# Kernel tuning notes

Hardware: AMD Instinct MI355X
Metric: run time of the kernel (lower is better)

## Reference

```python
import jax, jax.numpy as jnp
import numpy as np

BUFFER_C = 1.25

def setup_inputs() -> dict:
    key = jax.random.key(0)
    k1, k2, k3 = jax.random.split(key, 3)
    T, D, E = 4096, 1024, 8
    x = jax.random.normal(k1, (T, D), dtype=jnp.float32)
    Wg = jax.random.normal(k2, (D, E), dtype=jnp.float32) / np.sqrt(D)
    bg = jnp.zeros((E,), dtype=jnp.float32)
    W = jax.random.normal(k3, (E, D, D), dtype=jnp.float32) / np.sqrt(D)
    b = jnp.zeros((E, D), dtype=jnp.float32)
    return {"x": x, "Wg": Wg, "bg": bg, "W": W, "b": b}


def reference(x, Wg, bg, W, b):
    # Top-1 (Switch-style) routing with capacity buffer, per-expert Linear,
    # prob-weighted combine, plus load-balancing aux loss.
    T, D = x.shape
    E = W.shape[0]
    capacity = int(BUFFER_C * T / E)

    logits = x @ Wg + bg                      # [T, E]
    probs = jax.nn.softmax(logits, axis=-1)   # [T, E]
    top_idx = jnp.argmax(probs, axis=-1)      # [T]
    top_prob = jnp.take_along_axis(probs, top_idx[:, None], axis=-1)[:, 0]

    onehot = jax.nn.one_hot(top_idx, E, dtype=x.dtype)       # [T, E]
    # 1-indexed position of each token within its expert's buffer
    pos = jnp.cumsum(onehot, axis=0) * onehot                # [T, E]
    dispatch = jnp.where((onehot > 0) & (pos <= capacity), 1.0, 0.0).astype(x.dtype)

    # dense dispatch/combine equivalent of the masked per-expert loop
    xe = jnp.einsum('te,td->etd', dispatch, x)               # [E, T, D]
    ye = jnp.einsum('etd,edf->etf', xe, W) + b[:, None, :]   # [E, T, D]
    y = jnp.einsum('te,etf->tf', dispatch, ye)               # [T, D] (0 for dropped)
    out = y * top_prob[:, None]

    # aux load-balance loss: E * sum_e f_e * P_e
    f = onehot.mean(axis=0)
    P = probs.mean(axis=0)
    aux_loss = E * jnp.sum(f * P)
    return out, aux_loss
```

## Files before the change

kernel.cpp:

```cpp
#include <hip/hip_runtime.h>
#include <hip/hip_bf16.h>
#include <cstdint>

#define T_TOK 4096
#define D_DIM 1024
#define E_EXP 8
#define CAP   640
#define MAXDROP 3456
#define MT    10
#define GBLK  1024

typedef __attribute__((ext_vector_type(8))) short short8;
typedef __attribute__((ext_vector_type(4))) float f32x4;

__device__ inline unsigned short f2bf(float f) {
    uint32_t u = __float_as_uint(f);
    u += 0x7fffu + ((u >> 16) & 1u);
    return (unsigned short)(u >> 16);
}

__device__ inline void dma16(const void* g, void* l) {
    __builtin_amdgcn_global_load_lds(
        (const __attribute__((address_space(1))) unsigned int*)g,
        (__attribute__((address_space(3))) unsigned int*)l, 16, 0, 0);
}

#define WB_TILE(e, nt, kt) ((((size_t)(e) * 16 + (nt)) * 16 + (kt)) * 4096)
#define XG_TILE(e, mt, kt) ((((size_t)(e) * MT + (mt)) * 16 + (kt)) * 4096)

__global__ __launch_bounds__(256) void prep_kernel(
    const float* __restrict__ x, const float* __restrict__ Wg,
    const float* __restrict__ bg, const float* __restrict__ W,
    unsigned short* __restrict__ Wb,
    int* __restrict__ top_idx, float* __restrict__ top_prob,
    float* __restrict__ blkpart)
{
    int bid = blockIdx.x;
    int tid = threadIdx.x;

    if (bid >= GBLK) {
        __shared__ unsigned short tile[2][64][66];
        int bid2 = (bid - GBLK) * 2;
        int e   = bid2 >> 8;
        int kt  = (bid2 >> 4) & 15;
        int ntA = bid2 & 15;
        int k0  = kt * 64;
        int n0A = ntA * 64, n0B = n0A + 64;
        const float* Wsrc = W + (size_t)e * D_DIM * D_DIM;

        int rr = tid >> 4;
        int nn = (tid & 15) * 4;

        float4 r0[4], r1[4];
        #pragma unroll
        for (int p = 0; p < 4; p++)
            r0[p] = *(const float4*)(Wsrc + (size_t)(k0 + p * 16 + rr) * D_DIM + n0A + nn);
        #pragma unroll
        for (int p = 0; p < 4; p++) {
            ushort4 u;
            u.x = f2bf(r0[p].x); u.y = f2bf(r0[p].y); u.z = f2bf(r0[p].z); u.w = f2bf(r0[p].w);
            *(ushort4*)&tile[0][p * 16 + rr][nn] = u;
        }
        #pragma unroll
        for (int p = 0; p < 4; p++)
            r1[p] = *(const float4*)(Wsrc + (size_t)(k0 + p * 16 + rr) * D_DIM + n0B + nn);
        __syncthreads();
        {
            unsigned short* dst = Wb + WB_TILE(e, ntA, kt);
            #pragma unroll
            for (int p = 0; p < 2; p++) {
                int c = tid + 256 * p;
                int g = c >> 6, n = c & 63;
                short8 v;
                #pragma unroll
                for (int z = 0; z < 8; z++) v[z] = (short)tile[0][g * 8 + z][n];
                *(short8*)&dst[(size_t)c * 8] = v;
            }
        }
        #pragma unroll
        for (int p = 0; p < 4; p++) {
            ushort4 u;
            u.x = f2bf(r1[p].x); u.y = f2bf(r1[p].y); u.z = f2bf(r1[p].z); u.w = f2bf(r1[p].w);
            *(ushort4*)&tile[1][p * 16 + rr][nn] = u;
        }
        __syncthreads();
        {
            unsigned short* dst = Wb + WB_TILE(e, ntA + 1, kt);
            #pragma unroll
            for (int p = 0; p < 2; p++) {
                int c = tid + 256 * p;
                int g = c >> 6, n = c & 63;
                short8 v;
                #pragma unroll
                for (int z = 0; z < 8; z++) v[z] = (short)tile[1][g * 8 + z][n];
                *(short8*)&dst[(size_t)c * 8] = v;
            }
        }
    } else {
        __shared__ float probs_sm[4][8];
        int wid  = tid >> 6;
        int lane = tid & 63;
        int t = bid * 4 + wid;

        const float* xr = x + (size_t)t * D_DIM;

        float acc[8];
        #pragma unroll
        for (int e = 0; e < 8; e++) acc[e] = 0.f;

        #pragma unroll
        for (int ii = 0; ii < 16; ii++) {
            int d = lane + 64 * ii;
            float xv = xr[d];
            const float4* wr = (const float4*)(Wg + (size_t)d * 8);
            float4 a = wr[0], bq = wr[1];
            acc[0] += xv * a.x;  acc[1] += xv * a.y;
            acc[2] += xv * a.z;  acc[3] += xv * a.w;
            acc[4] += xv * bq.x; acc[5] += xv * bq.y;
            acc[6] += xv * bq.z; acc[7] += xv * bq.w;
        }
        #pragma unroll
        for (int off = 32; off > 0; off >>= 1) {
            #pragma unroll
            for (int e = 0; e < 8; e++) acc[e] += __shfl_xor(acc[e], off, 64);
        }
        if (lane == 0) {
            float lg[8];
            #pragma unroll
            for (int e = 0; e < 8; e++) lg[e] = acc[e] + bg[e];
            float m = lg[0]; int am = 0;
            #pragma unroll
            for (int e = 1; e < 8; e++) { if (lg[e] > m) { m = lg[e]; am = e; } }
            float ex[8], s = 0.f;
            #pragma unroll
            for (int e = 0; e < 8; e++) { ex[e] = __expf(lg[e] - m); s += ex[e]; }
            float inv = 1.f / s;
            top_idx[t]  = am;
            top_prob[t] = ex[am] * inv;
            #pragma unroll
            for (int e = 0; e < 8; e++) probs_sm[wid][e] = ex[e] * inv;
        }
        __syncthreads();
        if (tid < 8) {
            float s = probs_sm[0][tid] + probs_sm[1][tid]
                    + probs_sm[2][tid] + probs_sm[3][tid];
            blkpart[(size_t)bid * 8 + tid] = s;
        }
    }
}

__global__ __launch_bounds__(1024) void scan_kernel(
    const int* __restrict__ top_idx,
    int* __restrict__ tok_list, int* __restrict__ cnt,
    const float* __restrict__ blkpart,
    float* __restrict__ out, float* __restrict__ out_aux)
{
    __shared__ int counts[64][8];
    __shared__ int excl[64][8];
    __shared__ int fulltot[8];
    __shared__ int droplist[MAXDROP];
    __shared__ int ndrop;
    __shared__ float wpart[16][8];

    int tid  = threadIdx.x;
    int wv   = tid >> 6;
    int lane = tid & 63;
    unsigned long long ltmask = (lane == 0) ? 0ull : ((~0ull) >> (64 - lane));

    if (tid == 0) ndrop = 0;

    float p[8];
    {
        const float4* bp = (const float4*)(blkpart + (size_t)tid * 8);
        float4 p0 = bp[0], p1 = bp[1];
        p[0] = p0.x; p[1] = p0.y; p[2] = p0.z; p[3] = p0.w;
        p[4] = p1.x; p[5] = p1.y; p[6] = p1.z; p[7] = p1.w;
    }

    int ecache[4];
    #pragma unroll
    for (int c = 0; c < 4; c++)
        ecache[c] = top_idx[(4 * wv + c) * 64 + lane];

    #pragma unroll
    for (int c = 0; c < 4; c++) {
        int chunk = 4 * wv + c;
        int e = ecache[c];
        #pragma unroll
        for (int q = 0; q < 8; q++) {
            unsigned long long mk = __ballot(e == q);
            int tot = __popcll(mk);
            if (lane == q) counts[chunk][q] = tot;
        }
    }
    __syncthreads();

    if (wv == 0) {
        #pragma unroll
        for (int q = 0; q < 8; q++) {
            int v = counts[lane][q];
            int orig = v;
            #pragma unroll
            for (int off = 1; off < 64; off <<= 1) {
                int n = __shfl_up(v, off, 64);
                if (lane >= off) v += n;
            }
            excl[lane][q] = v - orig;
            int total = __shfl(v, 63, 64);
            if (lane == 0) {
                fulltot[q] = total;
                cnt[q] = total < CAP ? total : CAP;
            }
        }
    }
    __syncthreads();

    #pragma unroll
    for (int c = 0; c < 4; c++) {
        int chunk = 4 * wv + c;
        int t = chunk * 64 + lane;
        int e = ecache[c];
        int pos = 0;
        #pragma unroll
        for (int q = 0; q < 8; q++) {
            unsigned long long mk = __ballot(e == q);
            if (e == q) pos = excl[chunk][q] + __popcll(mk & ltmask);
        }
        if (pos < CAP) {
            tok_list[e * CAP + pos] = t;
        } else {
            int di = atomicAdd(&ndrop, 1);
            droplist[di] = t;
        }
    }

    #pragma unroll
    for (int off = 32; off > 0; off >>= 1) {
        #pragma unroll
        for (int e = 0; e < 8; e++) p[e] += __shfl_xor(p[e], off, 64);
    }
    if (lane == 0) {
        #pragma unroll
        for (int e = 0; e < 8; e++) wpart[wv][e] = p[e];
    }
    __syncthreads();

    int nd = ndrop;
    int grp = tid >> 8;
    int col = (tid & 255) * 4;
    float4 z = {0.f, 0.f, 0.f, 0.f};
    for (int d = grp; d < nd; d += 4) {
        int row = droplist[d];
        *(float4*)&out[(size_t)row * D_DIM + col] = z;
    }

    if (tid == 0) {
        float s = 0.f;
        #pragma unroll
        for (int e = 0; e < 8; e++) {
            float Pe = 0.f;
            #pragma unroll
            for (int w = 0; w < 16; w++) Pe += wpart[w][e];
            s += ((float)fulltot[e] / (float)T_TOK) * (Pe / (float)T_TOK);
        }
        out_aux[0] = (float)E_EXP * s;
    }
}

__global__ __launch_bounds__(256) void gather_kernel(
    const float* __restrict__ x, const int* __restrict__ tok_list,
    const int* __restrict__ cnt, unsigned short* __restrict__ xg)
{
    int bid = blockIdx.x;
    int e   = bid / (MT * 16);
    int rem = bid % (MT * 16);
    int mt  = rem >> 4, kt = rem & 15;
    int count = cnt[e];
    int m0 = mt * 64;
    if (m0 >= count) return;

    int tid = threadIdx.x;
    const int* tl = tok_list + e * CAP;
    unsigned short* dst = xg + XG_TILE(e, mt, kt);

    #pragma unroll
    for (int p = 0; p < 2; p++) {
        int c = tid + 256 * p;
        int g = c >> 6, row = c & 63;
        int gm = m0 + row;
        int tok = tl[gm < count ? gm : count - 1];
        const float* src = x + (size_t)tok * D_DIM + kt * 64 + g * 8;
        float4 v0 = *(const float4*)(src);
        float4 v1 = *(const float4*)(src + 4);
        short8 v;
        v[0] = f2bf(v0.x); v[1] = f2bf(v0.y); v[2] = f2bf(v0.z); v[3] = f2bf(v0.w);
        v[4] = f2bf(v1.x); v[5] = f2bf(v1.y); v[6] = f2bf(v1.z); v[7] = f2bf(v1.w);
        *(short8*)&dst[(size_t)c * 8] = v;
    }
}

__device__ inline void stage_dma(const unsigned short* gAt, const unsigned short* gBt,
                                 unsigned short (*Ab)[64][8], unsigned short (*Bb)[64][8],
                                 int w, int lane)
{
    size_t lo = (size_t)lane * 8;
    dma16(gAt + (size_t)w * 512 + lo,       &Ab[w][0][0]);
    dma16(gAt + (size_t)(w + 4) * 512 + lo, &Ab[w + 4][0][0]);
    dma16(gBt + (size_t)w * 512 + lo,       &Bb[w][0][0]);
    dma16(gBt + (size_t)(w + 4) * 512 + lo, &Bb[w + 4][0][0]);
}

__global__ __launch_bounds__(256) void expert_gemm(
    const unsigned short* __restrict__ xg, const unsigned short* __restrict__ Wb,
    const float* __restrict__ bias,
    const int* __restrict__ tok_list, const int* __restrict__ cnt,
    const float* __restrict__ top_prob, float* __restrict__ out)
{
    int bid = blockIdx.x;
    int e   = bid / (MT * 16);
    int rem = bid % (MT * 16);
    int mt  = rem >> 4, nt = rem & 15;
    int count = cnt[e];
    int m0 = mt * 64;
    if (m0 >= count) return;
    int n0 = nt * 64;

    __shared__ unsigned short Ab[2][8][64][8];
    __shared__ unsigned short Bb[2][8][64][8];

    int tid  = threadIdx.x;
    int lane = tid & 63, w = tid >> 6;
    int quad = lane >> 4, l16 = lane & 15;
    int mw = (w >> 1) * 32, nw = (w & 1) * 32;

    const int* tl = tok_list + e * CAP;
    const unsigned short* gA0 = xg + XG_TILE(e, mt, 0);
    const unsigned short* gB0 = Wb + WB_TILE(e, nt, 0);

    f32x4 acc[2][2];
    #pragma unroll
    for (int i = 0; i < 2; i++)
        #pragma unroll
        for (int j = 0; j < 2; j++)
            acc[i][j] = (f32x4){0.f, 0.f, 0.f, 0.f};

    stage_dma(gA0, gB0, Ab[0], Bb[0], w, lane);

    int cur = 0;
    #pragma unroll 1
    for (int kt = 0; kt < 16; kt++) {
        __syncthreads();
        if (kt + 1 < 16)
            stage_dma(gA0 + (size_t)(kt + 1) * 4096, gB0 + (size_t)(kt + 1) * 4096,
                      Ab[cur ^ 1], Bb[cur ^ 1], w, lane);

        short8 af[2][2], bf[2][2];
        #pragma unroll
        for (int s = 0; s < 2; s++) {
            #pragma unroll
            for (int i = 0; i < 2; i++) {
                af[s][i] = *(const short8*)&Ab[cur][s * 4 + quad][mw + 16 * i + l16][0];
                bf[s][i] = *(const short8*)&Bb[cur][s * 4 + quad][nw + 16 * i + l16][0];
            }
        }
        #pragma unroll
        for (int s = 0; s < 2; s++)
            #pragma unroll
            for (int i = 0; i < 2; i++)
                #pragma unroll
                for (int j = 0; j < 2; j++)
                    acc[i][j] = __builtin_amdgcn_mfma_f32_16x16x32_bf16(
                        af[s][i], bf[s][j], acc[i][j], 0, 0, 0);
        cur ^= 1;
    }

    float bv[2];
    #pragma unroll
    for (int j = 0; j < 2; j++)
        bv[j] = bias[e * D_DIM + n0 + nw + 16 * j + l16];

    #pragma unroll
    for (int i = 0; i < 2; i++) {
        int rb = m0 + mw + 16 * i + quad * 4;
        #pragma unroll
        for (int r = 0; r < 4; r++) {
            int gm = rb + r;
            if (gm >= count) continue;
            int tok = tl[gm];
            float p = top_prob[tok];
            float* orow = out + (size_t)tok * D_DIM + n0 + nw + l16;
            #pragma unroll
            for (int j = 0; j < 2; j++)
                orow[16 * j] = (acc[i][j][r] + bv[j]) * p;
        }
    }
}

extern "C" void kernel_launch(void* const* d_in, const int* in_sizes, int n_in,
                              void* d_out, int out_size, void* d_ws, size_t ws_size,
                              hipStream_t stream) {
    const float* x  = (const float*)d_in[0];
    const float* Wg = (const float*)d_in[1];
    const float* bg = (const float*)d_in[2];
    const float* W  = (const float*)d_in[3];
    const float* b  = (const float*)d_in[4];
    float* out = (float*)d_out;

    char* ws = (char*)d_ws;
    unsigned short* Wb = (unsigned short*)(ws + 0);
    unsigned short* xg = (unsigned short*)(ws + 16777216);
    int*   top_idx  = (int*)(ws + 27262976);
    float* top_prob = (float*)(ws + 27279360);
    int*   tok_list = (int*)(ws + 27295744);
    int*   cnt      = (int*)(ws + 27316224);
    float* blkpart  = (float*)(ws + 27316256);

    hipLaunchKernelGGL(prep_kernel, dim3(GBLK + 1024), dim3(256), 0, stream,
                       x, Wg, bg, W, Wb, top_idx, top_prob, blkpart);
    hipLaunchKernelGGL(scan_kernel, dim3(1), dim3(1024), 0, stream,
                       top_idx, tok_list, cnt, blkpart, out, out + (size_t)T_TOK * D_DIM);
    hipLaunchKernelGGL(gather_kernel, dim3(E_EXP * MT * 16), dim3(256), 0, stream,
                       x, tok_list, cnt, xg);
    hipLaunchKernelGGL(expert_gemm, dim3(E_EXP * MT * 16), dim3(256), 0, stream,
                       xg, Wb, b, tok_list, cnt, top_prob, out);
}
```

Measured before the change: 142.5 us.

## Fuse routing scan into prep and token gather into expert GEMM

The single-block scan kernel is folded into the tail of prep_kernel: an atomic done-counter picks the last routing block, which then builds the per-expert token lists, zeroes dropped rows and computes the aux loss. The separate gather kernel and its bf16 staging buffer are removed. expert_gemm now loads fp32 x rows directly through a token index kept in shared memory, converts them to bf16 in registers and writes them to LDS, with the next k-tile prefetched into registers. This drops two launches and a full write and read of the gathered activations. In exchange the scan runs on only 256 threads, and the smaller drop-list capacity assumes that few tokens overflow expert capacity.

```diff
diff --git a/kernel.cpp b/kernel.cpp
--- a/kernel.cpp
+++ b/kernel.cpp
@@ -6,7 +6,7 @@
 #define D_DIM 1024
 #define E_EXP 8
 #define CAP   640
-#define MAXDROP 3456
+#define MAXDROP 1024
 #define MT    10
 #define GBLK  1024
 
@@ -25,15 +25,23 @@
         (__attribute__((address_space(3))) unsigned int*)l, 16, 0, 0);
 }
 
+__device__ inline int agload_i(const int* p) {
+    return __hip_atomic_load(p, __ATOMIC_RELAXED, __HIP_MEMORY_SCOPE_AGENT);
+}
+__device__ inline float agload_f(const float* p) {
+    return __hip_atomic_load(p, __ATOMIC_RELAXED, __HIP_MEMORY_SCOPE_AGENT);
+}
+
 #define WB_TILE(e, nt, kt) ((((size_t)(e) * 16 + (nt)) * 16 + (kt)) * 4096)
-#define XG_TILE(e, mt, kt) ((((size_t)(e) * MT + (mt)) * 16 + (kt)) * 4096)
 
 __global__ __launch_bounds__(256) void prep_kernel(
     const float* __restrict__ x, const float* __restrict__ Wg,
     const float* __restrict__ bg, const float* __restrict__ W,
     unsigned short* __restrict__ Wb,
     int* __restrict__ top_idx, float* __restrict__ top_prob,
-    float* __restrict__ blkpart)
+    float* __restrict__ blkpart,
+    int* __restrict__ tok_list, int* __restrict__ cnt, int* __restrict__ done,
+    float* __restrict__ out, float* __restrict__ out_aux)
 {
     int bid = blockIdx.x;
     int tid = threadIdx.x;
@@ -96,8 +104,12 @@
                 *(short8*)&dst[(size_t)c * 8] = v;
             }
         }
-    } else {
-        __shared__ float probs_sm[4][8];
+        return;
+    }
+
+    __shared__ float probs_sm[4][8];
+    __shared__ int   is_last;
+    {
         int wid  = tid >> 6;
         int lane = tid & 63;
         int t = bid * 4 + wid;
@@ -147,22 +159,20 @@
             blkpart[(size_t)bid * 8 + tid] = s;
         }
     }
-}
-
-__global__ __launch_bounds__(1024) void scan_kernel(
-    const int* __restrict__ top_idx,
-    int* __restrict__ tok_list, int* __restrict__ cnt,
-    const float* __restrict__ blkpart,
-    float* __restrict__ out, float* __restrict__ out_aux)
-{
+
+    __threadfence();
+    __syncthreads();
+    if (tid == 0) is_last = (atomicAdd(done, 1) == GBLK - 1);
+    __syncthreads();
+    if (!is_last) return;
+
     __shared__ int counts[64][8];
     __shared__ int excl[64][8];
     __shared__ int fulltot[8];
     __shared__ int droplist[MAXDROP];
     __shared__ int ndrop;
-    __shared__ float wpart[16][8];
-
-    int tid  = threadIdx.x;
+    __shared__ float wpart[4][8];
+
     int wv   = tid >> 6;
     int lane = tid & 63;
     unsigned long long ltmask = (lane == 0) ? 0ull : ((~0ull) >> (64 - lane));
@@ -170,21 +180,23 @@
     if (tid == 0) ndrop = 0;
 
     float p[8];
-    {
-        const float4* bp = (const float4*)(blkpart + (size_t)tid * 8);
-        float4 p0 = bp[0], p1 = bp[1];
-        p[0] = p0.x; p[1] = p0.y; p[2] = p0.z; p[3] = p0.w;
-        p[4] = p1.x; p[5] = p1.y; p[6] = p1.z; p[7] = p1.w;
-    }
-
-    int ecache[4];
-    #pragma unroll
-    for (int c = 0; c < 4; c++)
-        ecache[c] = top_idx[(4 * wv + c) * 64 + lane];
-
-    #pragma unroll
-    for (int c = 0; c < 4; c++) {
-        int chunk = 4 * wv + c;
+    #pragma unroll
+    for (int e = 0; e < 8; e++) p[e] = 0.f;
+    #pragma unroll
+    for (int r = 0; r < 4; r++) {
+        const float* bp = blkpart + (size_t)(tid * 4 + r) * 8;
+        #pragma unroll
+        for (int e = 0; e < 8; e++) p[e] += agload_f(bp + e);
+    }
+
+    int ecache[16];
+    #pragma unroll
+    for (int c = 0; c < 16; c++)
+        ecache[c] = agload_i(top_idx + (wv * 16 + c) * 64 + lane);
+
+    #pragma unroll
+    for (int c = 0; c < 16; c++) {
+        int chunk = wv * 16 + c;
         int e = ecache[c];
         #pragma unroll
         for (int q = 0; q < 8; q++) {
@@ -216,8 +228,8 @@
     __syncthreads();
 
     #pragma unroll
-    for (int c = 0; c < 4; c++) {
-        int chunk = 4 * wv + c;
+    for (int c = 0; c < 16; c++) {
+        int chunk = wv * 16 + c;
         int t = chunk * 64 + lane;
         int e = ecache[c];
         int pos = 0;
@@ -246,72 +258,25 @@
     __syncthreads();
 
     int nd = ndrop;
-    int grp = tid >> 8;
-    int col = (tid & 255) * 4;
     float4 z = {0.f, 0.f, 0.f, 0.f};
-    for (int d = grp; d < nd; d += 4) {
+    for (int d = 0; d < nd; d++) {
         int row = droplist[d];
-        *(float4*)&out[(size_t)row * D_DIM + col] = z;
+        *(float4*)&out[(size_t)row * D_DIM + tid * 4] = z;
     }
 
     if (tid == 0) {
         float s = 0.f;
         #pragma unroll
         for (int e = 0; e < 8; e++) {
-            float Pe = 0.f;
-            #pragma unroll
-            for (int w = 0; w < 16; w++) Pe += wpart[w][e];
+            float Pe = wpart[0][e] + wpart[1][e] + wpart[2][e] + wpart[3][e];
             s += ((float)fulltot[e] / (float)T_TOK) * (Pe / (float)T_TOK);
         }
         out_aux[0] = (float)E_EXP * s;
     }
 }
 
-__global__ __launch_bounds__(256) void gather_kernel(
-    const float* __restrict__ x, const int* __restrict__ tok_list,
-    const int* __restrict__ cnt, unsigned short* __restrict__ xg)
-{
-    int bid = blockIdx.x;
-    int e   = bid / (MT * 16);
-    int rem = bid % (MT * 16);
-    int mt  = rem >> 4, kt = rem & 15;
-    int count = cnt[e];
-    int m0 = mt * 64;
-    if (m0 >= count) return;
-
-    int tid = threadIdx.x;
-    const int* tl = tok_list + e * CAP;
-    unsigned short* dst = xg + XG_TILE(e, mt, kt);
-
-    #pragma unroll
-    for (int p = 0; p < 2; p++) {
-        int c = tid + 256 * p;
-        int g = c >> 6, row = c & 63;
-        int gm = m0 + row;
-        int tok = tl[gm < count ? gm : count - 1];
-        const float* src = x + (size_t)tok * D_DIM + kt * 64 + g * 8;
-        float4 v0 = *(const float4*)(src);
-        float4 v1 = *(const float4*)(src + 4);
-        short8 v;
-        v[0] = f2bf(v0.x); v[1] = f2bf(v0.y); v[2] = f2bf(v0.z); v[3] = f2bf(v0.w);
-        v[4] = f2bf(v1.x); v[5] = f2bf(v1.y); v[6] = f2bf(v1.z); v[7] = f2bf(v1.w);
-        *(short8*)&dst[(size_t)c * 8] = v;
-    }
-}
-
-__device__ inline void stage_dma(const unsigned short* gAt, const unsigned short* gBt,
-                                 unsigned short (*Ab)[64][8], unsigned short (*Bb)[64][8],
-                                 int w, int lane)
-{
-    size_t lo = (size_t)lane * 8;
-    dma16(gAt + (size_t)w * 512 + lo,       &Ab[w][0][0]);
-    dma16(gAt + (size_t)(w + 4) * 512 + lo, &Ab[w + 4][0][0]);
-    dma16(gBt + (size_t)w * 512 + lo,       &Bb[w][0][0]);
-    dma16(gBt + (size_t)(w + 4) * 512 + lo, &Bb[w + 4][0][0]);
-}
-
 __global__ __launch_bounds__(256) void expert_gemm(
-    const unsigned short* __restrict__ xg, const unsigned short* __restrict__ Wb,
+    const float* __restrict__ x, const unsigned short* __restrict__ Wb,
     const float* __restrict__ bias,
     const int* __restrict__ tok_list, const int* __restrict__ cnt,
     const float* __restrict__ top_prob, float* __restrict__ out)
@@ -327,15 +292,42 @@
 
     __shared__ unsigned short Ab[2][8][64][8];
     __shared__ unsigned short Bb[2][8][64][8];
+    __shared__ int tok_sm[64];
 
     int tid  = threadIdx.x;
     int lane = tid & 63, w = tid >> 6;
     int quad = lane >> 4, l16 = lane & 15;
     int mw = (w >> 1) * 32, nw = (w & 1) * 32;
+    int arow = tid >> 2, aq = tid & 3;
 
     const int* tl = tok_list + e * CAP;
-    const unsigned short* gA0 = xg + XG_TILE(e, mt, 0);
-    const unsigned short* gB0 = Wb + WB_TILE(e, nt, 0);
+    if (tid < 64) { int gm = m0 + tid; tok_sm[tid] = tl[gm < count ? gm : count - 1]; }
+
+    const unsigned short* gB0 = Wb + WB_TILE(e, nt, 0) + (size_t)lane * 8;
+
+    #define DMAB(kt, buf) do {                                                \
+        const unsigned short* gb = gB0 + (size_t)(kt) * 4096;                 \
+        dma16(gb + (size_t)w * 512,       &Bb[buf][w][0][0]);                 \
+        dma16(gb + (size_t)(w + 4) * 512, &Bb[buf][w + 4][0][0]);             \
+    } while (0)
+
+    __syncthreads();
+    const float* xrow = x + (size_t)tok_sm[arow] * D_DIM + aq * 16;
+
+    float4 ra0, ra1, ra2, ra3;
+    #define XLOAD(ks) do {                                                    \
+        const float4* s_ = (const float4*)(xrow + (size_t)(ks) * 64);         \
+        ra0 = s_[0]; ra1 = s_[1]; ra2 = s_[2]; ra3 = s_[3];                   \
+    } while (0)
+    #define AWRITE(buf) do {                                                  \
+        short8 v_, u_;                                                        \
+        v_[0]=f2bf(ra0.x); v_[1]=f2bf(ra0.y); v_[2]=f2bf(ra0.z); v_[3]=f2bf(ra0.w); \
+        v_[4]=f2bf(ra1.x); v_[5]=f2bf(ra1.y); v_[6]=f2bf(ra1.z); v_[7]=f2bf(ra1.w); \
+        u_[0]=f2bf(ra2.x); u_[1]=f2bf(ra2.y); u_[2]=f2bf(ra2.z); u_[3]=f2bf(ra2.w); \
+        u_[4]=f2bf(ra3.x); u_[5]=f2bf(ra3.y); u_[6]=f2bf(ra3.z); u_[7]=f2bf(ra3.w); \
+        *(short8*)&Ab[buf][2 * aq][arow][0]     = v_;                         \
+        *(short8*)&Ab[buf][2 * aq + 1][arow][0] = u_;                         \
+    } while (0)
 
     f32x4 acc[2][2];
     #pragma unroll
@@ -344,15 +336,19 @@
         for (int j = 0; j < 2; j++)
             acc[i][j] = (f32x4){0.f, 0.f, 0.f, 0.f};
 
-    stage_dma(gA0, gB0, Ab[0], Bb[0], w, lane);
+    XLOAD(0); DMAB(0, 0);
+    AWRITE(0);
+    XLOAD(1);
+    __syncthreads();
 
     int cur = 0;
     #pragma unroll 1
     for (int kt = 0; kt < 16; kt++) {
-        __syncthreads();
-        if (kt + 1 < 16)
-            stage_dma(gA0 + (size_t)(kt + 1) * 4096, gB0 + (size_t)(kt + 1) * 4096,
-                      Ab[cur ^ 1], Bb[cur ^ 1], w, lane);
+        if (kt + 1 < 16) {
+            DMAB(kt + 1, cur ^ 1);
+            AWRITE(cur ^ 1);
+            if (kt + 2 < 16) XLOAD(kt + 2);
+        }
 
         short8 af[2][2], bf[2][2];
         #pragma unroll
@@ -371,8 +367,13 @@
                 for (int j = 0; j < 2; j++)
                     acc[i][j] = __builtin_amdgcn_mfma_f32_16x16x32_bf16(
                         af[s][i], bf[s][j], acc[i][j], 0, 0, 0);
+
+        __syncthreads();
         cur ^= 1;
     }
+    #undef XLOAD
+    #undef AWRITE
+    #undef DMAB
 
     float bv[2];
     #pragma unroll
@@ -386,7 +387,7 @@
         for (int r = 0; r < 4; r++) {
             int gm = rb + r;
             if (gm >= count) continue;
-            int tok = tl[gm];
+            int tok = tok_sm[gm - m0];
             float p = top_prob[tok];
             float* orow = out + (size_t)tok * D_DIM + n0 + nw + l16;
             #pragma unroll
@@ -408,19 +409,17 @@
 
     char* ws = (char*)d_ws;
     unsigned short* Wb = (unsigned short*)(ws + 0);
-    unsigned short* xg = (unsigned short*)(ws + 16777216);
-    int*   top_idx  = (int*)(ws + 27262976);
-    float* top_prob = (float*)(ws + 27279360);
-    int*   tok_list = (int*)(ws + 27295744);
-    int*   cnt      = (int*)(ws + 27316224);
-    float* blkpart  = (float*)(ws + 27316256);
-
+    int*   top_idx  = (int*)(ws + 16777216);
+    float* top_prob = (float*)(ws + 16793600);
+    int*   tok_list = (int*)(ws + 16809984);
+    int*   cnt      = (int*)(ws + 16830464);
+    float* blkpart  = (float*)(ws + 16830496);
+    int*   done     = (int*)(ws + 16863264);
+
+    hipMemsetAsync(done, 0, sizeof(int), stream);
     hipLaunchKernelGGL(prep_kernel, dim3(GBLK + 1024), dim3(256), 0, stream,
-                       x, Wg, bg, W, Wb, top_idx, top_prob, blkpart);
-    hipLaunchKernelGGL(scan_kernel, dim3(1), dim3(1024), 0, stream,
-                       top_idx, tok_list, cnt, blkpart, out, out + (size_t)T_TOK * D_DIM);
-    hipLaunchKernelGGL(gather_kernel, dim3(E_EXP * MT * 16), dim3(256), 0, stream,
-                       x, tok_list, cnt, xg);
+                       x, Wg, bg, W, Wb, top_idx, top_prob, blkpart,
+                       tok_list, cnt, done, out, out + (size_t)T_TOK * D_DIM);
     hipLaunchKernelGGL(expert_gemm, dim3(E_EXP * MT * 16), dim3(256), 0, stream,
-                       xg, Wb, b, tok_list, cnt, top_prob, out);
-}
+                       x, Wb, b, tok_list, cnt, top_prob, out);
+}
```

New measurement: 280.7 us. 97.0% more time.
